# Optimization experiments

Hardware: AMD Instinct MI355X
Metric: run time of the kernel (lower is better)

The kernel has to match this reference:

```python
import jax, jax.numpy as jnp
import numpy as np

T, B, S, H, E, V = 100, 64, 602, 1024, 512, 10000


def setup_inputs() -> dict:
    key = jax.random.key(0)
    ks = jax.random.split(key, 12)
    s = 0.02  # small init scale for numerical stability through tanh/sigmoid
    return {
        "tgt": jax.random.randint(ks[0], (T, B, 1), 0, V),
        "memory_bank": jax.random.normal(ks[1], (S, B, H), jnp.float32),
        "h0": jax.random.normal(ks[2], (2, B, H), jnp.float32) * 0.1,
        "c0": jax.random.normal(ks[3], (2, B, H), jnp.float32) * 0.1,
        "embedding": jax.random.normal(ks[4], (V, E), jnp.float32) * s,
        "Wi0": jax.random.normal(ks[5], (4 * H, E + H), jnp.float32) * s,
        "Wh0": jax.random.normal(ks[6], (4 * H, H), jnp.float32) * s,
        "bi0": jnp.zeros((4 * H,), jnp.float32),
        "bh0": jnp.zeros((4 * H,), jnp.float32),
        "Wi1": jax.random.normal(ks[7], (4 * H, H), jnp.float32) * s,
        "Wh1": jax.random.normal(ks[8], (4 * H, H), jnp.float32) * s,
        "bi1": jnp.zeros((4 * H,), jnp.float32),
        "bh1": jnp.zeros((4 * H,), jnp.float32),
        "W_attn": jax.random.normal(ks[9], (H, H), jnp.float32) * s,
        "W_out": jax.random.normal(ks[10], (H, 2 * H), jnp.float32) * s,
    }


def _lstm_cell(x, h, c, Wi, Wh, bi, bh):
    # PyTorch LSTM gate order: i, f, g, o
    g = x @ Wi.T + h @ Wh.T + bi + bh
    i, f, gg, o = jnp.split(g, 4, axis=-1)
    c2 = jax.nn.sigmoid(f) * c + jax.nn.sigmoid(i) * jnp.tanh(gg)
    h2 = jax.nn.sigmoid(o) * jnp.tanh(c2)
    return h2, c2


def reference(tgt, memory_bank, h0, c0, embedding, Wi0, Wh0, bi0, bh0,
              Wi1, Wh1, bi1, bh1, W_attn, W_out):
    emb = embedding[tgt[:, :, 0]]            # [T, B, E]
    M = jnp.transpose(memory_bank, (1, 0, 2))  # [B, S, H]

    def step(carry, e_t):
        hl0, hl1, cl0, cl1, feed = carry
        x = jnp.concatenate([e_t, feed], axis=-1)        # input feeding
        nh0, nc0 = _lstm_cell(x, hl0, cl0, Wi0, Wh0, bi0, bh0)
        nh1, nc1 = _lstm_cell(nh0, hl1, cl1, Wi1, Wh1, bi1, bh1)
        # GlobalAttention 'general': score = (h W) . m
        q = nh1 @ W_attn.T                                # [B, H]
        align = jnp.einsum('bh,bsh->bs', q, M)            # [B, S]
        a = jax.nn.softmax(align, axis=-1)
        ctx = jnp.einsum('bs,bsh->bh', a, M)              # [B, H]
        out = jnp.tanh(jnp.concatenate([ctx, nh1], -1) @ W_out.T)  # attn_h
        return (nh0, nh1, nc0, nc1, out), (out, a)

    init = (h0[0], h0[1], c0[0], c0[1], jnp.zeros((B, H), emb.dtype))
    (_, _, _, _, _), (outs, attns) = jax.lax.scan(step, init, emb)
    return outs, attns  # [T,B,H], [T,B,S]
```

## Files before the change

### kernel.cpp

```cpp
#include <hip/hip_runtime.h>


#define DI __device__ __forceinline__

typedef __attribute__((ext_vector_type(4))) short s4v;
typedef __attribute__((ext_vector_type(8))) short s8v;
typedef __attribute__((ext_vector_type(4))) float f4v;

DI float b2f(short u) {
  unsigned int x = ((unsigned int)(unsigned short)u) << 16;
  float f; __builtin_memcpy(&f, &x, 4); return f;
}
DI short f2b(float f) {
  unsigned int x; __builtin_memcpy(&x, &f, 4);
  return (short)((x + 0x7fffu + ((x >> 16) & 1u)) >> 16);
}
DI s8v cat8(s4v lo, s4v hi) {
  s8v r; r[0]=lo[0];r[1]=lo[1];r[2]=lo[2];r[3]=lo[3];
  r[4]=hi[0];r[5]=hi[1];r[6]=hi[2];r[7]=hi[3]; return r;
}
DI f4v mfma16(s8v a, s8v b, f4v c) {
  return __builtin_amdgcn_mfma_f32_16x16x32_bf16(a, b, c, 0, 0, 0);
}
DI float sigm(float x) { return 1.f / (1.f + __expf(-x)); }

DI unsigned long long ld64c(const void* p) {
  return __hip_atomic_load((const unsigned long long*)p, __ATOMIC_RELAXED,
                           __HIP_MEMORY_SCOPE_SYSTEM);
}
DI void st64c(void* p, unsigned long long v) {
  __hip_atomic_store((unsigned long long*)p, v, __ATOMIC_RELAXED,
                     __HIP_MEMORY_SCOPE_SYSTEM);
}
DI float ldfc(const float* p) {
  return __hip_atomic_load(p, __ATOMIC_RELAXED, __HIP_MEMORY_SCOPE_SYSTEM);
}
DI void stfc(float* p, float v) {
  __hip_atomic_store(p, v, __ATOMIC_RELAXED, __HIP_MEMORY_SCOPE_SYSTEM);
}
DI int ld32c(const int* p) {
  return __hip_atomic_load(p, __ATOMIC_RELAXED, __HIP_MEMORY_SCOPE_SYSTEM);
}
DI void st32c(int* p, int v) {
  __hip_atomic_store(p, v, __ATOMIC_RELAXED, __HIP_MEMORY_SCOPE_SYSTEM);
}
DI void st16c(short* p, short v) {
  asm volatile("global_store_short %0, %1, off sc0 sc1"
               :: "v"(p), "v"((unsigned int)(unsigned short)v) : "memory");
}
union U64S { unsigned long long u; short s[4]; };
union U64F { unsigned long long u; float f[2]; };


__global__ void cvt_bf16(const float* __restrict__ src, short* __restrict__ dst, long n8) {
  long i = (long)blockIdx.x * blockDim.x + threadIdx.x;
  long stride = (long)gridDim.x * blockDim.x;
  for (; i < n8; i += stride) {
    const float* s = src + i * 8;
    s8v o;
    #pragma unroll
    for (int j = 0; j < 8; ++j) o[j] = f2b(s[j]);
    *(s8v*)(dst + i * 8) = o;
  }
}

__global__ void pack_w(const float* __restrict__ WA, int Ka,
                       const float* __restrict__ WB, int Kb,
                       short* __restrict__ dst, int N, long total) {
  long i = (long)blockIdx.x * blockDim.x + threadIdx.x;
  long stride = (long)gridDim.x * blockDim.x;
  for (; i < total; i += stride) {
    int c = (int)(i & 3);
    long r = i >> 2;
    int n = (int)(r % N);
    int kt = (int)(r / N);
    int k = kt * 32 + c * 8;
    const float* s = (k < Ka) ? (WA + (size_t)n * Ka + k)
                              : (WB + (size_t)n * Kb + (k - Ka));
    s8v o;
    #pragma unroll
    for (int j = 0; j < 8; ++j) o[j] = f2b(s[j]);
    *(s8v*)(dst + r * 32 + c * 8) = o;
  }
}

__global__ __launch_bounds__(64) void emb_gather(const int* __restrict__ tgt,
                                                 const float* __restrict__ emb,
                                                 short* __restrict__ dst) {
  int tb = blockIdx.x;
  int idx = tgt[tb];
  const float* s = emb + (size_t)idx * 512 + threadIdx.x * 8;
  s8v o;
  #pragma unroll
  for (int j = 0; j < 8; ++j) o[j] = f2b(s[j]);
  *(s8v*)(dst + (size_t)tb * 512 + threadIdx.x * 8) = o;
}

__global__ void init_state(const float* __restrict__ h0, const float* __restrict__ c0,
                           short* __restrict__ h0r, short* __restrict__ h1r,
                           float* __restrict__ c0buf, float* __restrict__ c1buf,
                           short* __restrict__ feedr) {
  int i = blockIdx.x * 256 + threadIdx.x;
  if (i < 65536) {
    h0r[i] = f2b(h0[i]);
    h1r[i] = f2b(h0[65536 + i]);
    int row = i >> 10, col = i & 1023;
    size_t coff = (size_t)((row >> 4) * 64 + (col >> 4)) * 256
                + (row & 15) * 16 + (col & 15);
    c0buf[coff] = c0[i];
    c1buf[coff] = c0[65536 + i];
    feedr[i] = 0;
  }
}


template <int NG>
DI void kloop(const short* __restrict__ A, int ld, int nkt,
              const short* __restrict__ Wp, size_t wkt,
              f4v* acc, int rA, int g) {
  if (nkt <= 0) return;
  const short* ap = A + (size_t)rA * ld + 4 * g;
  s4v alo = *(const s4v*)ap, ahi = *(const s4v*)(ap + 16);
  s4v blo[NG], bhi[NG];
  #pragma unroll
  for (int t = 0; t < NG; ++t) {
    blo[t] = *(const s4v*)(Wp + (size_t)t * 32768);
    bhi[t] = *(const s4v*)(Wp + (size_t)t * 32768 + 16);
  }
  for (int kt = 0; kt < nkt - 1; ++kt) {
    const short* apn = ap + (kt + 1) * 32;
    const short* bpn = Wp + (size_t)(kt + 1) * wkt;
    s4v nalo = *(const s4v*)apn, nahi = *(const s4v*)(apn + 16);
    s4v nblo[NG], nbhi[NG];
    #pragma unroll
    for (int t = 0; t < NG; ++t) {
      nblo[t] = *(const s4v*)(bpn + (size_t)t * 32768);
      nbhi[t] = *(const s4v*)(bpn + (size_t)t * 32768 + 16);
    }
    s8v a = cat8(alo, ahi);
    #pragma unroll
    for (int t = 0; t < NG; ++t) acc[t] = mfma16(a, cat8(blo[t], bhi[t]), acc[t]);
    alo = nalo; ahi = nahi;
    #pragma unroll
    for (int t = 0; t < NG; ++t) { blo[t] = nblo[t]; bhi[t] = nbhi[t]; }
  }
  s8v a = cat8(alo, ahi);
  #pragma unroll
  for (int t = 0; t < NG; ++t) acc[t] = mfma16(a, cat8(blo[t], bhi[t]), acc[t]);
}

template <int NG>
DI void seg_gemm(const short* __restrict__ A0, int ld0, int n0,
                 const short* __restrict__ A1, int ld1, int n1,
                 const short* __restrict__ A2, int ld2, int n2,
                 const short* __restrict__ wbase, size_t wkt,
                 int k0, int k1, f4v* acc, int rA, int g) {
  int s = 0;
  {
    int a = k0 > s ? k0 : s, b = k1 < (s + n0) ? k1 : (s + n0);
    if (a < b) kloop<NG>(A0 + (size_t)(a - s) * 32, ld0, b - a,
                         wbase + (size_t)a * wkt, wkt, acc, rA, g);
    s += n0;
  }
  {
    int a = k0 > s ? k0 : s, b = k1 < (s + n1) ? k1 : (s + n1);
    if (a < b) kloop<NG>(A1 + (size_t)(a - s) * 32, ld1, b - a,
                         wbase + (size_t)a * wkt, wkt, acc, rA, g);
    s += n1;
  }
  if (n2 > 0) {
    int a = k0 > s ? k0 : s, b = k1 < (s + n2) ? k1 : (s + n2);
    if (a < b) kloop<NG>(A2 + (size_t)(a - s) * 32, ld2, b - a,
                         wbase + (size_t)a * wkt, wkt, acc, rA, g);
  }
}

template <int NG>
DI void wave_reduce(f4v* acc, float* smem, int w, int l) {
  #pragma unroll
  for (int t4 = 0; t4 < NG; ++t4)
    *(f4v*)&smem[(w * 64 + l) * 20 + t4 * 4] = acc[t4];
  __syncthreads();
  if (w == 0) {
    #pragma unroll
    for (int t4 = 0; t4 < NG; ++t4) {
      f4v s0 = *(f4v*)&smem[l * 20 + t4 * 4];
      #pragma unroll
      for (int ww = 1; ww < 4; ++ww) {
        f4v v = *(f4v*)&smem[(ww * 64 + l) * 20 + t4 * 4];
        #pragma unroll
        for (int j = 0; j < 4; ++j) s0[j] += v[j];
      }
      acc[t4] = s0;
    }
  }
}


DI void gbar(int* bar, int bid, int want) {
  __syncthreads();
  int tid = threadIdx.x;
  if (bid == 0) {
    for (;;) {
      int ok = 1;
      if (tid > 0) ok = (ld32c(bar + tid * 16) >= want);
      if (__syncthreads_and(ok)) break;
      __builtin_amdgcn_s_sleep(1);
    }
    if (tid == 0) st32c(bar + 4096, want);
  } else {
    if (tid == 0) {
      st32c(bar + bid * 16, want);
      while (ld32c(bar + 4096) < want) __builtin_amdgcn_s_sleep(2);
    }
  }
  __syncthreads();
}


__global__ __launch_bounds__(256, 1) void decoder_k(
    const short* __restrict__ W0p, const short* __restrict__ W1p,
    const short* __restrict__ Wop, const short* __restrict__ Wap,
    const short* __restrict__ emba,
    const float* __restrict__ bi0, const float* __restrict__ bh0,
    const float* __restrict__ bi1, const float* __restrict__ bh1,
    short* h0r, short* h1r, short* feedr, short* ctxr, short* qb,
    float* c0b, float* c1b, float* alg, float* part, float* csum,
    const short* __restrict__ Mb, const float* __restrict__ memf,
    float* out, int useMb, int* bar) {
  __shared__ float smem[5248];
  const int bid = blockIdx.x, tid = threadIdx.x;
  const int w = tid >> 6, l = tid & 63, r15 = l & 15, g = l >> 4;
  const int cs = bid & 63, rt = bid >> 6;
  int barno = 0;
  f4v z = {0.f, 0.f, 0.f, 0.f};

  for (int t = 0; t < 100; ++t) {
    const size_t scur = (size_t)t * 65536, snxt = (size_t)(t + 1) * 65536;

    {
      f4v acc[4] = {z, z, z, z};
      const short* wbase = W0p + (size_t)(cs * 16 + r15) * 32 + 4 * g;
      seg_gemm<4>(emba + (size_t)t * 64 * 512, 512, 16,
                  feedr + scur, 1024, 32, h0r + scur, 1024, 32,
                  wbase, (size_t)4096 * 32, w * 20, w * 20 + 20,
                  acc, rt * 16 + r15, g);
      wave_reduce<4>(acc, smem, w, l);
      if (w == 0) {
        int h = cs * 16 + r15;
        float bs0 = bi0[h] + bh0[h];
        float bs1 = bi0[1024 + h] + bh0[1024 + h];
        float bs2 = bi0[2048 + h] + bh0[2048 + h];
        float bs3 = bi0[3072 + h] + bh0[3072 + h];
        #pragma unroll
        for (int q = 0; q < 4; ++q) {
          int brow = rt * 16 + g * 4 + q;
          size_t off = (size_t)brow * 1024 + h;
          size_t coff = (size_t)bid * 256 + (g * 4 + q) * 16 + r15;
          float iv = acc[0][q] + bs0, fv = acc[1][q] + bs1;
          float gv = acc[2][q] + bs2, ov = acc[3][q] + bs3;
          float cn = sigm(fv) * c0b[coff] + sigm(iv) * tanhf(gv);
          float hn = sigm(ov) * tanhf(cn);
          c0b[coff] = cn;
          st16c(h0r + snxt + off, f2b(hn));
        }
      }
      gbar(bar, bid, ++barno);
    }

    {
      f4v acc[4] = {z, z, z, z};
      const short* wbase = W1p + (size_t)(cs * 16 + r15) * 32 + 4 * g;
      seg_gemm<4>(h0r + snxt, 1024, 32, h1r + scur, 1024, 32,
                  (const short*)nullptr, 0, 0,
                  wbase, (size_t)4096 * 32, w * 16, w * 16 + 16,
                  acc, rt * 16 + r15, g);
      wave_reduce<4>(acc, smem, w, l);
      if (w == 0) {
        int h = cs * 16 + r15;
        float bs0 = bi1[h] + bh1[h];
        float bs1 = bi1[1024 + h] + bh1[1024 + h];
        float bs2 = bi1[2048 + h] + bh1[2048 + h];
        float bs3 = bi1[3072 + h] + bh1[3072 + h];
        #pragma unroll
        for (int q = 0; q < 4; ++q) {
          int brow = rt * 16 + g * 4 + q;
          size_t off = (size_t)brow * 1024 + h;
          size_t coff = (size_t)bid * 256 + (g * 4 + q) * 16 + r15;
          float iv = acc[0][q] + bs0, fv = acc[1][q] + bs1;
          float gv = acc[2][q] + bs2, ov = acc[3][q] + bs3;
          float cn = sigm(fv) * c1b[coff] + sigm(iv) * tanhf(gv);
          float hn = sigm(ov) * tanhf(cn);
          c1b[coff] = cn;
          st16c(h1r + snxt + off, f2b(hn));
        }
      }
      gbar(bar, bid, ++barno);
    }

    {
      f4v acc[1] = {z};
      const short* wbase = Wap + (size_t)(cs * 16 + r15) * 32 + 4 * g;
      seg_gemm<1>(h1r + snxt, 1024, 32, (const short*)nullptr, 0, 0,
                  (const short*)nullptr, 0, 0,
                  wbase, (size_t)1024 * 32, w * 8, w * 8 + 8,
                  acc, rt * 16 + r15, g);
      wave_reduce<1>(acc, smem, w, l);
      if (w == 0) {
        int nb = cs * 16 + r15;
        #pragma unroll
        for (int q = 0; q < 4; ++q) {
          int brow = rt * 16 + g * 4 + q;
          st16c(qb + (size_t)brow * 1024 + nb, f2b(acc[0][q]));
        }
      }
      gbar(bar, bid, ++barno);
    }

    {
      int b = bid & 63, chunk = bid >> 6;
      int s0 = chunk * 151;
      int send = 602 < s0 + 151 ? 602 : s0 + 151;
      const short* qp = qb + (size_t)b * 1024 + l * 16;
      float qf[16];
      #pragma unroll
      for (int c4 = 0; c4 < 4; ++c4) {
        U64S x; x.u = ld64c(qp + c4 * 4);
        #pragma unroll
        for (int j = 0; j < 4; ++j) qf[c4 * 4 + j] = b2f(x.s[j]);
      }
      float o[16];
      #pragma unroll
      for (int j = 0; j < 16; ++j) o[j] = 0.f;
      float ls8 = 0.f;
      for (int s = s0 + w; s < send; s += 16) {
        int sr[4] = {s, s + 4, s + 8, s + 12};
        bool has[4];
        #pragma unroll
        for (int r = 0; r < 4; ++r) has[r] = sr[r] < send;
        float mv[4][16];
        if (useMb) {
          #pragma unroll
          for (int r = 0; r < 4; ++r) {
            int sx = has[r] ? sr[r] : s;
            const short* mp = Mb + ((size_t)sx * 64 + b) * 1024 + l * 16;
            s8v a0 = *(const s8v*)mp, a1 = *(const s8v*)(mp + 8);
            #pragma unroll
            for (int j = 0; j < 8; ++j) {
              mv[r][j] = b2f(a0[j]); mv[r][8 + j] = b2f(a1[j]);
            }
          }
        } else {
          #pragma unroll
          for (int r = 0; r < 4; ++r) {
            int sx = has[r] ? sr[r] : s;
            const float* mp = memf + ((size_t)sx * 64 + b) * 1024 + l * 16;
            f4v a0 = *(const f4v*)mp, a1 = *(const f4v*)(mp + 4);
            f4v a2 = *(const f4v*)(mp + 8), a3 = *(const f4v*)(mp + 12);
            #pragma unroll
            for (int j = 0; j < 4; ++j) {
              mv[r][j] = a0[j]; mv[r][4 + j] = a1[j];
              mv[r][8 + j] = a2[j]; mv[r][12 + j] = a3[j];
            }
          }
        }
        float d[4] = {0.f, 0.f, 0.f, 0.f};
        #pragma unroll
        for (int j = 0; j < 16; ++j) {
          #pragma unroll
          for (int r = 0; r < 4; ++r) d[r] += qf[j] * mv[r][j];
        }
        #pragma unroll
        for (int off = 32; off; off >>= 1) {
          #pragma unroll
          for (int r = 0; r < 4; ++r) d[r] += __shfl_down(d[r], off);
        }
        float p[4];
        #pragma unroll
        for (int r = 0; r < 4; ++r) {
          d[r] = __shfl(d[r], 0);
          p[r] = has[r] ? __expf(fminf(d[r], 80.f) - 8.f) : 0.f;
          ls8 += p[r];
        }
        if (l == 0) {
          #pragma unroll
          for (int r = 0; r < 4; ++r)
            if (has[r]) stfc(alg + b * 602 + sr[r], p[r]);
        }
        #pragma unroll
        for (int j = 0; j < 16; ++j)
          o[j] += p[0] * mv[0][j] + p[1] * mv[1][j]
                + p[2] * mv[2][j] + p[3] * mv[3][j];
      }
      float* pp = part + (size_t)(b * 16 + chunk * 4 + w) * 1024;
      #pragma unroll
      for (int j4 = 0; j4 < 8; ++j4) {
        U64F x; x.f[0] = o[j4 * 2]; x.f[1] = o[j4 * 2 + 1];
        st64c(pp + l * 16 + j4 * 2, x.u);
      }
      if (l == 0) smem[5120 + w] = ls8;
      __syncthreads();
      if (tid == 0)
        stfc(csum + b * 4 + chunk,
             smem[5120] + smem[5121] + smem[5122] + smem[5123]);
      __syncthreads();
      if (tid == 0) {
        int* acnt = bar + 4352 + b * 16;
        __hip_atomic_fetch_add(acnt, 1, __ATOMIC_RELAXED,
                               __HIP_MEMORY_SCOPE_AGENT);
        while (__hip_atomic_load(acnt, __ATOMIC_RELAXED,
                                 __HIP_MEMORY_SCOPE_AGENT) < 4 * (t + 1))
          __builtin_amdgcn_s_sleep(1);
      }
      __syncthreads();
      {
        const float* cs4 = csum + b * 4;
        float L8 = ldfc(cs4) + ldfc(cs4 + 1) + ldfc(cs4 + 2) + ldfc(cs4 + 3);
        float invL = 1.f / L8;
        if (tid < 128) {
          int h = chunk * 256 + tid * 2;
          float a0 = 0.f, a1 = 0.f;
          #pragma unroll
          for (int p = 0; p < 16; ++p) {
            U64F x; x.u = ld64c(part + (size_t)(b * 16 + p) * 1024 + h);
            a0 += x.f[0]; a1 += x.f[1];
          }
          short* cp = ctxr + snxt + (size_t)b * 1024 + h;
          st16c(cp, f2b(a0 * invL));
          st16c(cp + 1, f2b(a1 * invL));
        }
        float* attns = out + 6553600 + (size_t)t * 64 * 602;
        for (int i = s0 + tid; i < send; i += 256)
          stfc(attns + b * 602 + i, ldfc(alg + b * 602 + i) * invL);
      }
      gbar(bar, bid, ++barno);
    }

    {
      f4v acc[1] = {z};
      const short* wbase = Wop + (size_t)(cs * 16 + r15) * 32 + 4 * g;
      seg_gemm<1>(ctxr + snxt, 1024, 32, h1r + snxt, 1024, 32,
                  (const short*)nullptr, 0, 0,
                  wbase, (size_t)1024 * 32, w * 16, w * 16 + 16,
                  acc, rt * 16 + r15, g);
      wave_reduce<1>(acc, smem, w, l);
      if (w == 0) {
        int nb = cs * 16 + r15;
        float* outp = out + (size_t)t * 65536;
        #pragma unroll
        for (int q = 0; q < 4; ++q) {
          int brow = rt * 16 + g * 4 + q;
          size_t off = (size_t)brow * 1024 + nb;
          float v = tanhf(acc[0][q]);
          stfc(outp + off, v);
          st16c(feedr + snxt + off, f2b(v));
        }
      }
      gbar(bar, bid, ++barno);
    }
  }
}


extern "C" void kernel_launch(void* const* d_in, const int* in_sizes, int n_in,
                              void* d_out, int out_size, void* d_ws, size_t ws_size,
                              hipStream_t stream) {
  const int*   tgt  = (const int*)  d_in[0];
  const float* mem  = (const float*)d_in[1];
  const float* h0   = (const float*)d_in[2];
  const float* c0   = (const float*)d_in[3];
  const float* embw = (const float*)d_in[4];
  const float* Wi0  = (const float*)d_in[5];
  const float* Wh0  = (const float*)d_in[6];
  const float* bi0  = (const float*)d_in[7];
  const float* bh0  = (const float*)d_in[8];
  const float* Wi1  = (const float*)d_in[9];
  const float* Wh1  = (const float*)d_in[10];
  const float* bi1  = (const float*)d_in[11];
  const float* bh1  = (const float*)d_in[12];
  const float* Wat  = (const float*)d_in[13];
  const float* Wou  = (const float*)d_in[14];
  float* out = (float*)d_out;

  char* base = (char*)d_ws;
  size_t off = 0;
  auto alloc = [&](size_t bytes) -> void* {
    void* p = base + off;
    off += (bytes + 255) & ~(size_t)255;
    return p;
  };
  const size_t RING = (size_t)101 * 65536;
  int* bar = (int*)alloc(32768);
  short* qb   = (short*)alloc(65536 * 2);
  float* csum = (float*)alloc(64 * 4 * 4);
  float* c0b  = (float*)alloc(65536 * 4);
  float* c1b  = (float*)alloc(65536 * 4);
  float* alg  = (float*)alloc((size_t)64 * 602 * 4);
  float* part = (float*)alloc((size_t)64 * 16 * 1024 * 4);
  short* emba = (short*)alloc((size_t)100 * 64 * 512 * 2);
  short* Wap  = (short*)alloc((size_t)32 * 1024 * 32 * 2);
  short* Wop  = (short*)alloc((size_t)64 * 1024 * 32 * 2);
  short* W1p  = (short*)alloc((size_t)64 * 4096 * 32 * 2);
  short* W0p  = (short*)alloc((size_t)80 * 4096 * 32 * 2);
  short* h0r  = (short*)alloc(RING * 2);
  short* h1r  = (short*)alloc(RING * 2);
  short* feedr= (short*)alloc(RING * 2);
  short* ctxr = (short*)alloc(RING * 2);
  const size_t MBE = (size_t)602 * 64 * 1024;
  bool useMb = (off + MBE * 2 + 256) <= ws_size;
  short* Mb = useMb ? (short*)alloc(MBE * 2) : nullptr;

  hipMemsetAsync(bar, 0, 32768, stream);
  hipLaunchKernelGGL(emb_gather, dim3(6400), dim3(64), 0, stream, tgt, embw, emba);
  hipLaunchKernelGGL(pack_w, dim3(2048), dim3(256), 0, stream, Wi0, 1536, Wh0, 1024,
                     W0p, 4096, (long)80 * 4096 * 4);
  hipLaunchKernelGGL(pack_w, dim3(2048), dim3(256), 0, stream, Wi1, 1024, Wh1, 1024,
                     W1p, 4096, (long)64 * 4096 * 4);
  hipLaunchKernelGGL(pack_w, dim3(1024), dim3(256), 0, stream, Wou, 2048, Wou, 2048,
                     Wop, 1024, (long)64 * 1024 * 4);
  hipLaunchKernelGGL(pack_w, dim3(512), dim3(256), 0, stream, Wat, 1024, Wat, 1024,
                     Wap, 1024, (long)32 * 1024 * 4);
  hipLaunchKernelGGL(init_state, dim3(256), dim3(256), 0, stream, h0, c0,
                     h0r, h1r, c0b, c1b, feedr);
  if (useMb)
    hipLaunchKernelGGL(cvt_bf16, dim3(2048), dim3(256), 0, stream, mem, Mb,
                       (long)(MBE / 8));

  hipLaunchKernelGGL(decoder_k, dim3(256), dim3(256), 0, stream,
                     W0p, W1p, Wop, Wap, emba,
                     bi0, bh0, bi1, bh1,
                     h0r, h1r, feedr, ctxr, qb,
                     c0b, c1b, alg, part, csum,
                     Mb, mem, out, (int)useMb,
                     bar);
}
```

Baseline: 7.607 ms.

## Replace global grid barriers with per-row-group dataflow flags between phases

```diff
diff --git a/kernel.cpp b/kernel.cpp
--- a/kernel.cpp
+++ b/kernel.cpp
@@ -197,24 +197,24 @@
 }
 
 
-DI void gbar(int* bar, int bid, int want) {
-  __syncthreads();
-  int tid = threadIdx.x;
-  if (bid == 0) {
-    for (;;) {
-      int ok = 1;
-      if (tid > 0) ok = (ld32c(bar + tid * 16) >= want);
-      if (__syncthreads_and(ok)) break;
-      __builtin_amdgcn_s_sleep(1);
-    }
-    if (tid == 0) st32c(bar + 4096, want);
-  } else {
-    if (tid == 0) {
-      st32c(bar + bid * 16, want);
-      while (ld32c(bar + 4096) < want) __builtin_amdgcn_s_sleep(2);
-    }
-  }
-  __syncthreads();
+DI void post(int* slot, int val) {
+  if (threadIdx.x == 0) st32c(slot, val);
+}
+DI void wait64(const int* slots, int want) {
+  for (;;) {
+    int ok = 1;
+    if (threadIdx.x < 64) ok = (ld32c(slots + threadIdx.x * 16) >= want);
+    if (__syncthreads_and(ok)) break;
+    __builtin_amdgcn_s_sleep(4);
+  }
+}
+DI void wait4(const int* slots, int want) {
+  for (;;) {
+    int ok = 1;
+    if (threadIdx.x < 4) ok = (ld32c(slots + threadIdx.x * 16) >= want);
+    if (__syncthreads_and(ok)) break;
+    __builtin_amdgcn_s_sleep(2);
+  }
 }
 
 
@@ -232,13 +232,22 @@
   const int bid = blockIdx.x, tid = threadIdx.x;
   const int w = tid >> 6, l = tid & 63, r15 = l & 15, g = l >> 4;
   const int cs = bid & 63, rt = bid >> 6;
-  int barno = 0;
+  const int b = bid & 63, chunk = bid >> 6;
+  int* s_p1 = bar;
+  int* s_p2 = bar + 4096;
+  int* s_p3 = bar + 8192;
+  int* s_p6 = bar + 12288;
+  int* s_p4 = bar + 16384;
+  int* s_mg = bar + 20480;
+  int* my_gemm_slot = bar ;
   f4v z = {0.f, 0.f, 0.f, 0.f};
+  (void)my_gemm_slot;
 
   for (int t = 0; t < 100; ++t) {
     const size_t scur = (size_t)t * 65536, snxt = (size_t)(t + 1) * 65536;
 
     {
+      wait64(s_p6 + rt * 1024, t);
       f4v acc[4] = {z, z, z, z};
       const short* wbase = W0p + (size_t)(cs * 16 + r15) * 32 + 4 * g;
       seg_gemm<4>(emba + (size_t)t * 64 * 512, 512, 16,
@@ -265,10 +274,12 @@
           st16c(h0r + snxt + off, f2b(hn));
         }
       }
-      gbar(bar, bid, ++barno);
+      __syncthreads();
+      post(s_p1 + (rt * 64 + cs) * 16, t + 1);
     }
 
     {
+      wait64(s_p1 + rt * 1024, t + 1);
       f4v acc[4] = {z, z, z, z};
       const short* wbase = W1p + (size_t)(cs * 16 + r15) * 32 + 4 * g;
       seg_gemm<4>(h0r + snxt, 1024, 32, h1r + scur, 1024, 32,
@@ -295,10 +306,12 @@
           st16c(h1r + snxt + off, f2b(hn));
         }
       }
-      gbar(bar, bid, ++barno);
+      __syncthreads();
+      post(s_p2 + (rt * 64 + cs) * 16, t + 1);
     }
 
     {
+      wait64(s_p2 + rt * 1024, t + 1);
       f4v acc[1] = {z};
       const short* wbase = Wap + (size_t)(cs * 16 + r15) * 32 + 4 * g;
       seg_gemm<1>(h1r + snxt, 1024, 32, (const short*)nullptr, 0, 0,
@@ -314,11 +327,13 @@
           st16c(qb + (size_t)brow * 1024 + nb, f2b(acc[0][q]));
         }
       }
-      gbar(bar, bid, ++barno);
+      __syncthreads();
+      post(s_p3 + (rt * 64 + cs) * 16, t + 1);
     }
 
     {
-      int b = bid & 63, chunk = bid >> 6;
+      wait64(s_p3 + (b >> 4) * 1024, t + 1);
+      wait4(s_mg + b * 64, t);
       int s0 = chunk * 151;
       int send = 602 < s0 + 151 ? 602 : s0 + 151;
       const short* qp = qb + (size_t)b * 1024 + l * 16;
@@ -404,15 +419,8 @@
         stfc(csum + b * 4 + chunk,
              smem[5120] + smem[5121] + smem[5122] + smem[5123]);
       __syncthreads();
-      if (tid == 0) {
-        int* acnt = bar + 4352 + b * 16;
-        __hip_atomic_fetch_add(acnt, 1, __ATOMIC_RELAXED,
-                               __HIP_MEMORY_SCOPE_AGENT);
-        while (__hip_atomic_load(acnt, __ATOMIC_RELAXED,
-                                 __HIP_MEMORY_SCOPE_AGENT) < 4 * (t + 1))
-          __builtin_amdgcn_s_sleep(1);
-      }
-      __syncthreads();
+      post(s_p4 + (b * 4 + chunk) * 16, t + 1);
+      wait4(s_p4 + b * 64, t + 1);
       {
         const float* cs4 = csum + b * 4;
         float L8 = ldfc(cs4) + ldfc(cs4 + 1) + ldfc(cs4 + 2) + ldfc(cs4 + 3);
@@ -433,10 +441,12 @@
         for (int i = s0 + tid; i < send; i += 256)
           stfc(attns + b * 602 + i, ldfc(alg + b * 602 + i) * invL);
       }
-      gbar(bar, bid, ++barno);
+      __syncthreads();
+      post(s_mg + (b * 4 + chunk) * 16, t + 1);
     }
 
     {
+      wait64(s_mg + rt * 1024, t + 1);
       f4v acc[1] = {z};
       const short* wbase = Wop + (size_t)(cs * 16 + r15) * 32 + 4 * g;
       seg_gemm<1>(ctxr + snxt, 1024, 32, h1r + snxt, 1024, 32,
@@ -456,7 +466,8 @@
           st16c(feedr + snxt + off, f2b(v));
         }
       }
-      gbar(bar, bid, ++barno);
+      __syncthreads();
+      post(s_p6 + (rt * 64 + cs) * 16, t + 1);
     }
   }
 }
@@ -490,7 +501,7 @@
     return p;
   };
   const size_t RING = (size_t)101 * 65536;
-  int* bar = (int*)alloc(32768);
+  int* bar = (int*)alloc(131072);
   short* qb   = (short*)alloc(65536 * 2);
   float* csum = (float*)alloc(64 * 4 * 4);
   float* c0b  = (float*)alloc(65536 * 4);
@@ -510,7 +521,7 @@
   bool useMb = (off + MBE * 2 + 256) <= ws_size;
   short* Mb = useMb ? (short*)alloc(MBE * 2) : nullptr;
 
-  hipMemsetAsync(bar, 0, 32768, stream);
+  hipMemsetAsync(bar, 0, 131072, stream);
   hipLaunchKernelGGL(emb_gather, dim3(6400), dim3(64), 0, stream, tgt, embw, emba);
   hipLaunchKernelGGL(pack_w, dim3(2048), dim3(256), 0, stream, Wi0, 1536, Wh0, 1024,
                      W0p, 4096, (long)80 * 4096 * 4);
```

Result: faster. 7.353 ms (-3.4%).
